# Kernel optimization log

Measured on AMD Instinct MI355X. Metric: run time of the kernel, lower is better.

Reference implementation:

```python
import jax, jax.numpy as jnp
import numpy as np

NUM_USER = 100000
NUM_ITEM = 150000
NUM_NODES = NUM_USER + NUM_ITEM
NUM_EDGES = 4000000
DIM = 64
N_LAYERS = 3
LAYER_PERM = (2, 0, 1)  # idx = [2, 0, 1] in the torch source


def setup_inputs() -> dict:
    key = jax.random.key(0)
    k1, k2 = jax.random.split(key)
    edge_index = jax.random.randint(k1, (2, NUM_EDGES), 0, NUM_NODES, dtype=jnp.int32)
    emb = jax.random.normal(k2, (NUM_NODES, DIM), dtype=jnp.float32) * 0.01  # nn.init.normal_(std=0.01)
    return {"edge_index": edge_index, "emb": emb}


def _spmm(row, col, val, feat, n):
    # out[r] = sum_{e: row[e]==r} val[e] * feat[col[e]]  -- gather + segment scatter-add
    return jax.ops.segment_sum(val[:, None] * feat[col], row, num_segments=n)


def reference(edge_index, emb):
    n = emb.shape[0]
    row, col = edge_index[0], edge_index[1]
    # dropout_node: edge-value dropout (identity in eval) + add_self_loop + bi-norm
    loop = jnp.arange(n, dtype=edge_index.dtype)
    row = jnp.concatenate([row, loop])
    col = jnp.concatenate([col, loop])
    val = jnp.ones(row.shape[0], dtype=emb.dtype)
    deg = jax.ops.segment_sum(val, row, num_segments=n)
    d_inv_sqrt = jnp.where(deg > 0, jax.lax.rsqrt(jnp.maximum(deg, 1e-12)), 0.0).astype(emb.dtype)
    val = val * d_inv_sqrt[row] * d_inv_sqrt[col]  # D^-1/2 A D^-1/2
    # n_layers of LightGCN-style SpMM propagation
    feat = emb
    feats = []
    for _ in range(N_LAYERS):
        feat = _spmm(row, col, val, feat, n)
        feats.append(feat)
    all_feat = jnp.stack(feats, axis=1)[:, jnp.array(LAYER_PERM), :]  # [N, L, D]
    return all_feat, feat
```

## Files before the change

### kernel.cpp

```cpp
#include <hip/hip_runtime.h>
#include <hip/hip_fp16.h>

#define N_NODES 250000
#define N_EDGES 4000000
#define DIM 64

#define RB_BITS 9
#define ROWS_PER_B 512
#define NB 489
#define NBPAD 512
#define P1_CHUNK 8192
#define P1_THREADS 512
#define P2_THREADS 512
#define P2_CAP 13312

#define WS_FP16_NEED 84000000ull

__device__ __forceinline__ unsigned pack2h(float a, float b) {
    unsigned ua = (unsigned)__half_as_ushort(__float2half_rn(a));
    unsigned ub = (unsigned)__half_as_ushort(__float2half_rn(b));
    return ua | (ub << 16);
}
__device__ __forceinline__ float2 unpack2h(unsigned u) {
    float a = __half2float(__ushort_as_half((unsigned short)(u & 0xffffu)));
    float b = __half2float(__ushort_as_half((unsigned short)(u >> 16)));
    return make_float2(a, b);
}

__global__ __launch_bounds__(256) void bucket_count(const int* __restrict__ row,
                                                    int* __restrict__ bcnt) {
    __shared__ int h[NBPAD];
    for (int i = threadIdx.x; i < NBPAD; i += 256) h[i] = 0;
    __syncthreads();
    int stride = gridDim.x * 256;
    for (int e4 = blockIdx.x * 256 + threadIdx.x; e4 < N_EDGES / 4; e4 += stride) {
        int4 r = ((const int4*)row)[e4];
        atomicAdd(&h[r.x >> RB_BITS], 1);
        atomicAdd(&h[r.y >> RB_BITS], 1);
        atomicAdd(&h[r.z >> RB_BITS], 1);
        atomicAdd(&h[r.w >> RB_BITS], 1);
    }
    __syncthreads();
    for (int i = threadIdx.x; i < NB; i += 256) {
        int v = h[i];
        if (v) atomicAdd(&bcnt[i], v);
    }
}

__global__ __launch_bounds__(NBPAD) void scan_buckets(const int* __restrict__ bcnt,
                                                      int* __restrict__ bbase,
                                                      int* __restrict__ bcur) {
    __shared__ int sm[NBPAD];
    int t = threadIdx.x;
    int v = (t < NB) ? bcnt[t] : 0;
    sm[t] = v;
    __syncthreads();
    for (int off = 1; off < NBPAD; off <<= 1) {
        int u = (t >= off) ? sm[t - off] : 0;
        __syncthreads();
        sm[t] += u;
        __syncthreads();
    }
    int ex = sm[t] - v;
    if (t < NB) { bbase[t] = ex; bcur[t] = ex; }
}

__global__ __launch_bounds__(P1_THREADS) void partition_edges(
        const int* __restrict__ row, const int* __restrict__ col,
        int* __restrict__ bcur, unsigned int* __restrict__ bucketed) {
    __shared__ int histo[NBPAD];
    __shared__ int base[NBPAD];
    __shared__ int cursor[NBPAD];
    __shared__ int gbase[NBPAD];
    __shared__ unsigned int staged[P1_CHUNK];
    __shared__ unsigned short stagedB[P1_CHUNK];

    int t = threadIdx.x;
    histo[t] = 0;
    __syncthreads();

    int c4base = blockIdx.x * (P1_CHUNK / 4);
    int4 r[4], c[4];
    bool val[4];
#pragma unroll
    for (int i = 0; i < 4; ++i) {
        int e4 = c4base + i * P1_THREADS + t;
        val[i] = (e4 < N_EDGES / 4);
        if (val[i]) {
            r[i] = ((const int4*)row)[e4];
            c[i] = ((const int4*)col)[e4];
            atomicAdd(&histo[r[i].x >> RB_BITS], 1);
            atomicAdd(&histo[r[i].y >> RB_BITS], 1);
            atomicAdd(&histo[r[i].z >> RB_BITS], 1);
            atomicAdd(&histo[r[i].w >> RB_BITS], 1);
        }
    }
    __syncthreads();
    int hv = histo[t];
    base[t] = hv;
    __syncthreads();
    for (int off = 1; off < NBPAD; off <<= 1) {
        int u = (t >= off) ? base[t - off] : 0;
        __syncthreads();
        base[t] += u;
        __syncthreads();
    }
    int ex = base[t] - hv;
    base[t] = ex;
    cursor[t] = ex;
    if (t < NB && hv > 0) gbase[t] = atomicAdd(&bcur[t], hv);
    __syncthreads();
#pragma unroll
    for (int i = 0; i < 4; ++i) {
        if (val[i]) {
            int rr[4] = {r[i].x, r[i].y, r[i].z, r[i].w};
            int cc[4] = {c[i].x, c[i].y, c[i].z, c[i].w};
#pragma unroll
            for (int u = 0; u < 4; ++u) {
                int b = rr[u] >> RB_BITS;
                int pos = atomicAdd(&cursor[b], 1);
                staged[pos]  = ((unsigned)(rr[u] & (ROWS_PER_B - 1)) << 18) | (unsigned)cc[u];
                stagedB[pos] = (unsigned short)b;
            }
        }
    }
    __syncthreads();
    int cnt_total = N_EDGES - blockIdx.x * P1_CHUNK;
    if (cnt_total > P1_CHUNK) cnt_total = P1_CHUNK;
    for (int s = t; s < cnt_total; s += P1_THREADS) {
        int b = stagedB[s];
        int gpos = gbase[b] + (s - base[b]);
        bucketed[gpos] = staged[s];
    }
}

__global__ __launch_bounds__(P2_THREADS) void build_csr(
        const int* __restrict__ bcnt, const int* __restrict__ bbase,
        unsigned int* csr,
        int* __restrict__ deg, int* __restrict__ row_ptr, float* __restrict__ dis) {
    __shared__ unsigned int staged[P2_CAP];
    __shared__ int histo[ROWS_PER_B];
    __shared__ int base[ROWS_PER_B];
    int b = blockIdx.x;
    int nb = bcnt[b];
    int gstart = bbase[b];
    int t = threadIdx.x;
    histo[t] = 0;
    __syncthreads();
    for (int s = t; s < nb; s += P2_THREADS) {
        unsigned int w = csr[gstart + s];
        staged[s] = w;
        atomicAdd(&histo[w >> 18], 1);
    }
    __syncthreads();
    int hv = histo[t];
    base[t] = hv;
    __syncthreads();
    for (int off = 1; off < ROWS_PER_B; off <<= 1) {
        int u = (t >= off) ? base[t - off] : 0;
        __syncthreads();
        base[t] += u;
        __syncthreads();
    }
    int ex = base[t] - hv;
    base[t] = ex;
    int node = (b << RB_BITS) + t;
    if (node < N_NODES) {
        deg[node] = hv;
        row_ptr[node] = gstart + ex;
        dis[node] = rsqrtf((float)(hv + 1));
    }
    __syncthreads();
    for (int s = t; s < nb; s += P2_THREADS) {
        unsigned int w = staged[s];
        int rl = (int)(w >> 18);
        int p = atomicAdd(&base[rl], 1);
        csr[gstart + p] = w & 0x3FFFFu;
    }
}

__global__ __launch_bounds__(256) void f32_to_f16(const float* __restrict__ in,
                                                  unsigned int* __restrict__ outh) {
    int i = blockIdx.x * blockDim.x + threadIdx.x;
    if (i < N_NODES * (DIM / 4)) {
        float4 v = ((const float4*)in)[i];
        uint2 pk;
        pk.x = pack2h(v.x, v.y);
        pk.y = pack2h(v.z, v.w);
        ((uint2*)outh)[i] = pk;
    }
}

__global__ __launch_bounds__(256) void spmm_h(const int* __restrict__ row_ptr,
                                              const int* __restrict__ deg,
                                              const int* __restrict__ csr_col,
                                              const float* __restrict__ dis,
                                              const unsigned int* __restrict__ fin_h,
                                              float* __restrict__ fout, int out_stride4, int out_off,
                                              unsigned int* __restrict__ fout_h,
                                              float* __restrict__ fout2) {
    int lane = threadIdx.x & 63;
    int lq   = lane & 15;
    int qb   = lane & 48;
    int r    = blockIdx.x * 16 + (threadIdx.x >> 4);
    if (r >= N_NODES) return;

    const uint2* fin2 = (const uint2*)fin_h;
    float dr = dis[r];
    uint2 sh = fin2[(size_t)r * 16 + lq];
    float2 s0 = unpack2h(sh.x), s1 = unpack2h(sh.y);
    float4 acc;
    acc.x = dr * s0.x; acc.y = dr * s0.y;
    acc.z = dr * s1.x; acc.w = dr * s1.y;

    int start = row_ptr[r];
    int cnt   = deg[r];
    for (int base = 0; base < cnt; base += 16) {
        int m = cnt - base; if (m > 16) m = 16;
        int cl = 0; float wl = 0.f;
        if (lq < m) {
            cl = csr_col[start + base + lq];
            wl = dis[cl];
        }
        int m4 = (m + 3) & ~3;
        for (int j = 0; j < m4; j += 4) {
            int c[4]; float w[4]; uint2 f[4];
#pragma unroll
            for (int u = 0; u < 4; ++u) {
                c[u] = __shfl(cl, qb + j + u);
                w[u] = __shfl(wl, qb + j + u);
                f[u] = fin2[(size_t)c[u] * 16 + lq];
            }
#pragma unroll
            for (int u = 0; u < 4; ++u) {
                float2 a = unpack2h(f[u].x), b = unpack2h(f[u].y);
                acc.x += w[u] * a.x;
                acc.y += w[u] * a.y;
                acc.z += w[u] * b.x;
                acc.w += w[u] * b.y;
            }
        }
    }
    float4 v;
    v.x = dr * acc.x; v.y = dr * acc.y;
    v.z = dr * acc.z; v.w = dr * acc.w;
    ((float4*)(fout + out_off))[(size_t)r * out_stride4 + lq] = v;
    if (fout_h) {
        uint2 pk;
        pk.x = pack2h(v.x, v.y);
        pk.y = pack2h(v.z, v.w);
        ((uint2*)fout_h)[(size_t)r * 16 + lq] = pk;
    }
    if (fout2) ((float4*)fout2)[(size_t)r * 16 + lq] = v;
}

__global__ __launch_bounds__(256) void spmm(const int* __restrict__ row_ptr,
                                            const int* __restrict__ deg,
                                            const int* __restrict__ csr_col,
                                            const float* __restrict__ dis,
                                            const float* __restrict__ fin, int in_stride4, int in_off,
                                            float* __restrict__ fout, int out_stride4, int out_off,
                                            float* __restrict__ fout2) {
    int lane = threadIdx.x & 63;
    int lq   = lane & 15;
    int qb   = lane & 48;
    int r    = blockIdx.x * 16 + (threadIdx.x >> 4);
    if (r >= N_NODES) return;

    const float4* fin4 = (const float4*)(fin + in_off);
    float dr = dis[r];
    float4 self = fin4[(size_t)r * in_stride4 + lq];
    float4 acc;
    acc.x = dr * self.x; acc.y = dr * self.y;
    acc.z = dr * self.z; acc.w = dr * self.w;

    int start = row_ptr[r];
    int cnt   = deg[r];
    for (int base = 0; base < cnt; base += 16) {
        int m = cnt - base; if (m > 16) m = 16;
        int cl = 0; float wl = 0.f;
        if (lq < m) {
            cl = csr_col[start + base + lq];
            wl = dis[cl];
        }
        int m4 = (m + 3) & ~3;
        for (int j = 0; j < m4; j += 4) {
            int c[4]; float w[4]; float4 f[4];
#pragma unroll
            for (int u = 0; u < 4; ++u) {
                c[u] = __shfl(cl, qb + j + u);
                w[u] = __shfl(wl, qb + j + u);
                f[u] = fin4[(size_t)c[u] * in_stride4 + lq];
            }
#pragma unroll
            for (int u = 0; u < 4; ++u) {
                acc.x += w[u] * f[u].x;
                acc.y += w[u] * f[u].y;
                acc.z += w[u] * f[u].z;
                acc.w += w[u] * f[u].w;
            }
        }
    }
    float4 v;
    v.x = dr * acc.x; v.y = dr * acc.y;
    v.z = dr * acc.z; v.w = dr * acc.w;
    ((float4*)(fout + out_off))[(size_t)r * out_stride4 + lq] = v;
    if (fout2) ((float4*)fout2)[(size_t)r * 16 + lq] = v;
}

extern "C" void kernel_launch(void* const* d_in, const int* in_sizes, int n_in,
                              void* d_out, int out_size, void* d_ws, size_t ws_size,
                              hipStream_t stream) {
    const int*   ei  = (const int*)d_in[0];
    const float* emb = (const float*)d_in[1];
    const int* row = ei;
    const int* col = ei + N_EDGES;
    float* out = (float*)d_out;

    char* ws = (char*)d_ws;
    int*   deg      = (int*)(ws + 0);
    int*   row_ptr  = (int*)(ws + 1000000);
    float* dis      = (float*)(ws + 2000000);
    int*   bcnt     = (int*)(ws + 3000000);
    int*   bbase    = (int*)(ws + 3002048);
    int*   bcur     = (int*)(ws + 3004096);
    unsigned int* csr = (unsigned int*)(ws + 4000000);
    unsigned int* bufA = (unsigned int*)(ws + 20000000);
    unsigned int* bufB = (unsigned int*)(ws + 52000000);

    hipMemsetAsync(bcnt, 0, NBPAD * sizeof(int), stream);

    bucket_count   <<<512, 256, 0, stream>>>(row, bcnt);
    scan_buckets   <<<1, NBPAD, 0, stream>>>(bcnt, bbase, bcur);
    int p1_blocks = (N_EDGES + P1_CHUNK - 1) / P1_CHUNK;
    partition_edges<<<p1_blocks, P1_THREADS, 0, stream>>>(row, col, bcur, csr);
    build_csr      <<<NB, P2_THREADS, 0, stream>>>(bcnt, bbase, csr, deg, row_ptr, dis);

    int spmm_blocks = N_NODES / 16 + 1;
    if (ws_size >= WS_FP16_NEED) {
        int cvt_blocks = (N_NODES * (DIM / 4) + 255) / 256;
        f32_to_f16<<<cvt_blocks, 256, 0, stream>>>(emb, bufB);
        spmm_h<<<spmm_blocks, 256, 0, stream>>>(row_ptr, deg, (const int*)csr, dis,
                                                bufB, out, 48, DIM, bufA, nullptr);
        spmm_h<<<spmm_blocks, 256, 0, stream>>>(row_ptr, deg, (const int*)csr, dis,
                                                bufA, out, 48, 2 * DIM, bufB, nullptr);
        spmm_h<<<spmm_blocks, 256, 0, stream>>>(row_ptr, deg, (const int*)csr, dis,
                                                bufB, out, 48, 0, nullptr, out + 48000000);
    } else {
        spmm<<<spmm_blocks, 256, 0, stream>>>(row_ptr, deg, (const int*)csr, dis,
                                              emb, 16, 0, out, 48, DIM, nullptr);
        spmm<<<spmm_blocks, 256, 0, stream>>>(row_ptr, deg, (const int*)csr, dis,
                                              out, 48, DIM, out, 48, 2 * DIM, nullptr);
        spmm<<<spmm_blocks, 256, 0, stream>>>(row_ptr, deg, (const int*)csr, dis,
                                              out, 48, 2 * DIM, out, 48, 0, out + 48000000);
    }
}
```

Before: 634.8 us.

## Use fixed-capacity bucket windows to drop the count/scan pass, unroll gathers by eight

Each row bucket now gets a fixed window of WCAP slots in an edge buffer, with cursors preset to b*WCAP. This removes the separate bucket_count pass, the scan, the memset and their launches. build_csr now reads the bucket window straight from global memory instead of staging it in LDS, and writes an out-of-place CSR buffer, which needs extra workspace. The fp16 SpMM inner gather loop is unrolled to 8 neighbours for more memory-level parallelism. The fixed windows assume no bucket exceeds 16384 edges, which holds for uniform random edges but would silently corrupt data if a bucket overflowed. The larger workspace requirement may also push execution onto the fp32 fallback.

```diff
diff --git a/kernel.cpp b/kernel.cpp
--- a/kernel.cpp
+++ b/kernel.cpp
@@ -8,13 +8,12 @@
 #define RB_BITS 9
 #define ROWS_PER_B 512
 #define NB 489
-#define NBPAD 512
+#define WCAP 16384
 #define P1_CHUNK 8192
 #define P1_THREADS 512
 #define P2_THREADS 512
-#define P2_CAP 13312
-
-#define WS_FP16_NEED 84000000ull
+
+#define WS_FP16_NEED 134000000ull
 
 __device__ __forceinline__ unsigned pack2h(float a, float b) {
     unsigned ua = (unsigned)__half_as_ushort(__float2half_rn(a));
@@ -27,51 +26,18 @@
     return make_float2(a, b);
 }
 
-__global__ __launch_bounds__(256) void bucket_count(const int* __restrict__ row,
-                                                    int* __restrict__ bcnt) {
-    __shared__ int h[NBPAD];
-    for (int i = threadIdx.x; i < NBPAD; i += 256) h[i] = 0;
-    __syncthreads();
-    int stride = gridDim.x * 256;
-    for (int e4 = blockIdx.x * 256 + threadIdx.x; e4 < N_EDGES / 4; e4 += stride) {
-        int4 r = ((const int4*)row)[e4];
-        atomicAdd(&h[r.x >> RB_BITS], 1);
-        atomicAdd(&h[r.y >> RB_BITS], 1);
-        atomicAdd(&h[r.z >> RB_BITS], 1);
-        atomicAdd(&h[r.w >> RB_BITS], 1);
-    }
-    __syncthreads();
-    for (int i = threadIdx.x; i < NB; i += 256) {
-        int v = h[i];
-        if (v) atomicAdd(&bcnt[i], v);
-    }
-}
-
-__global__ __launch_bounds__(NBPAD) void scan_buckets(const int* __restrict__ bcnt,
-                                                      int* __restrict__ bbase,
-                                                      int* __restrict__ bcur) {
-    __shared__ int sm[NBPAD];
+__global__ __launch_bounds__(512) void init_cursors(int* __restrict__ bcur) {
     int t = threadIdx.x;
-    int v = (t < NB) ? bcnt[t] : 0;
-    sm[t] = v;
-    __syncthreads();
-    for (int off = 1; off < NBPAD; off <<= 1) {
-        int u = (t >= off) ? sm[t - off] : 0;
-        __syncthreads();
-        sm[t] += u;
-        __syncthreads();
-    }
-    int ex = sm[t] - v;
-    if (t < NB) { bbase[t] = ex; bcur[t] = ex; }
+    if (t < NB) bcur[t] = t * WCAP;
 }
 
 __global__ __launch_bounds__(P1_THREADS) void partition_edges(
         const int* __restrict__ row, const int* __restrict__ col,
-        int* __restrict__ bcur, unsigned int* __restrict__ bucketed) {
-    __shared__ int histo[NBPAD];
-    __shared__ int base[NBPAD];
-    __shared__ int cursor[NBPAD];
-    __shared__ int gbase[NBPAD];
+        int* __restrict__ bcur, unsigned int* __restrict__ ebuf) {
+    __shared__ int histo[ROWS_PER_B];
+    __shared__ int base[ROWS_PER_B];
+    __shared__ int cursor[ROWS_PER_B];
+    __shared__ int gbase[ROWS_PER_B];
     __shared__ unsigned int staged[P1_CHUNK];
     __shared__ unsigned short stagedB[P1_CHUNK];
 
@@ -99,7 +65,7 @@
     int hv = histo[t];
     base[t] = hv;
     __syncthreads();
-    for (int off = 1; off < NBPAD; off <<= 1) {
+    for (int off = 1; off < ROWS_PER_B; off <<= 1) {
         int u = (t >= off) ? base[t - off] : 0;
         __syncthreads();
         base[t] += u;
@@ -130,28 +96,25 @@
     for (int s = t; s < cnt_total; s += P1_THREADS) {
         int b = stagedB[s];
         int gpos = gbase[b] + (s - base[b]);
-        bucketed[gpos] = staged[s];
+        ebuf[gpos] = staged[s];
     }
 }
 
 __global__ __launch_bounds__(P2_THREADS) void build_csr(
-        const int* __restrict__ bcnt, const int* __restrict__ bbase,
-        unsigned int* csr,
+        const int* __restrict__ bcur, const unsigned int* __restrict__ ebuf,
+        unsigned int* __restrict__ cbuf,
         int* __restrict__ deg, int* __restrict__ row_ptr, float* __restrict__ dis) {
-    __shared__ unsigned int staged[P2_CAP];
     __shared__ int histo[ROWS_PER_B];
     __shared__ int base[ROWS_PER_B];
     int b = blockIdx.x;
-    int nb = bcnt[b];
-    int gstart = bbase[b];
+    int wstart = b * WCAP;
+    int nb = bcur[b] - wstart;
+    const unsigned int* ewin = ebuf + wstart;
     int t = threadIdx.x;
     histo[t] = 0;
     __syncthreads();
-    for (int s = t; s < nb; s += P2_THREADS) {
-        unsigned int w = csr[gstart + s];
-        staged[s] = w;
-        atomicAdd(&histo[w >> 18], 1);
-    }
+    for (int s = t; s < nb; s += P2_THREADS)
+        atomicAdd(&histo[ewin[s] >> 18], 1);
     __syncthreads();
     int hv = histo[t];
     base[t] = hv;
@@ -167,15 +130,14 @@
     int node = (b << RB_BITS) + t;
     if (node < N_NODES) {
         deg[node] = hv;
-        row_ptr[node] = gstart + ex;
+        row_ptr[node] = wstart + ex;
         dis[node] = rsqrtf((float)(hv + 1));
     }
     __syncthreads();
     for (int s = t; s < nb; s += P2_THREADS) {
-        unsigned int w = staged[s];
-        int rl = (int)(w >> 18);
-        int p = atomicAdd(&base[rl], 1);
-        csr[gstart + p] = w & 0x3FFFFu;
+        unsigned int w = ewin[s];
+        int p = atomicAdd(&base[w >> 18], 1);
+        cbuf[wstart + p] = w & 0x3FFFFu;
     }
 }
 
@@ -193,7 +155,7 @@
 
 __global__ __launch_bounds__(256) void spmm_h(const int* __restrict__ row_ptr,
                                               const int* __restrict__ deg,
-                                              const int* __restrict__ csr_col,
+                                              const unsigned int* __restrict__ csr_col,
                                               const float* __restrict__ dis,
                                               const unsigned int* __restrict__ fin_h,
                                               float* __restrict__ fout, int out_stride4, int out_off,
@@ -219,25 +181,25 @@
         int m = cnt - base; if (m > 16) m = 16;
         int cl = 0; float wl = 0.f;
         if (lq < m) {
-            cl = csr_col[start + base + lq];
+            cl = (int)csr_col[start + base + lq];
             wl = dis[cl];
         }
-        int m4 = (m + 3) & ~3;
-        for (int j = 0; j < m4; j += 4) {
-            int c[4]; float w[4]; uint2 f[4];
-#pragma unroll
-            for (int u = 0; u < 4; ++u) {
+        int m8 = (m + 7) & ~7;
+        for (int j = 0; j < m8; j += 8) {
+            int c[8]; float w[8]; uint2 f[8];
+#pragma unroll
+            for (int u = 0; u < 8; ++u) {
                 c[u] = __shfl(cl, qb + j + u);
                 w[u] = __shfl(wl, qb + j + u);
                 f[u] = fin2[(size_t)c[u] * 16 + lq];
             }
 #pragma unroll
-            for (int u = 0; u < 4; ++u) {
-                float2 a = unpack2h(f[u].x), b = unpack2h(f[u].y);
+            for (int u = 0; u < 8; ++u) {
+                float2 a = unpack2h(f[u].x), bb = unpack2h(f[u].y);
                 acc.x += w[u] * a.x;
                 acc.y += w[u] * a.y;
-                acc.z += w[u] * b.x;
-                acc.w += w[u] * b.y;
+                acc.z += w[u] * bb.x;
+                acc.w += w[u] * bb.y;
             }
         }
     }
@@ -256,7 +218,7 @@
 
 __global__ __launch_bounds__(256) void spmm(const int* __restrict__ row_ptr,
                                             const int* __restrict__ deg,
-                                            const int* __restrict__ csr_col,
+                                            const unsigned int* __restrict__ csr_col,
                                             const float* __restrict__ dis,
                                             const float* __restrict__ fin, int in_stride4, int in_off,
                                             float* __restrict__ fout, int out_stride4, int out_off,
@@ -280,7 +242,7 @@
         int m = cnt - base; if (m > 16) m = 16;
         int cl = 0; float wl = 0.f;
         if (lq < m) {
-            cl = csr_col[start + base + lq];
+            cl = (int)csr_col[start + base + lq];
             wl = dis[cl];
         }
         int m4 = (m + 3) & ~3;
@@ -321,37 +283,33 @@
     int*   deg      = (int*)(ws + 0);
     int*   row_ptr  = (int*)(ws + 1000000);
     float* dis      = (float*)(ws + 2000000);
-    int*   bcnt     = (int*)(ws + 3000000);
-    int*   bbase    = (int*)(ws + 3002048);
-    int*   bcur     = (int*)(ws + 3004096);
-    unsigned int* csr = (unsigned int*)(ws + 4000000);
-    unsigned int* bufA = (unsigned int*)(ws + 20000000);
-    unsigned int* bufB = (unsigned int*)(ws + 52000000);
-
-    hipMemsetAsync(bcnt, 0, NBPAD * sizeof(int), stream);
-
-    bucket_count   <<<512, 256, 0, stream>>>(row, bcnt);
-    scan_buckets   <<<1, NBPAD, 0, stream>>>(bcnt, bbase, bcur);
+    int*   bcur     = (int*)(ws + 3000000);
+    unsigned int* ebuf = (unsigned int*)(ws + 4000000);
+    unsigned int* cbuf = (unsigned int*)(ws + 37000000);
+    unsigned int* bufA = (unsigned int*)(ws + 70000000);
+    unsigned int* bufB = (unsigned int*)(ws + 102000000);
+
+    init_cursors   <<<1, 512, 0, stream>>>(bcur);
     int p1_blocks = (N_EDGES + P1_CHUNK - 1) / P1_CHUNK;
-    partition_edges<<<p1_blocks, P1_THREADS, 0, stream>>>(row, col, bcur, csr);
-    build_csr      <<<NB, P2_THREADS, 0, stream>>>(bcnt, bbase, csr, deg, row_ptr, dis);
+    partition_edges<<<p1_blocks, P1_THREADS, 0, stream>>>(row, col, bcur, ebuf);
+    build_csr      <<<NB, P2_THREADS, 0, stream>>>(bcur, ebuf, cbuf, deg, row_ptr, dis);
 
     int spmm_blocks = N_NODES / 16 + 1;
     if (ws_size >= WS_FP16_NEED) {
         int cvt_blocks = (N_NODES * (DIM / 4) + 255) / 256;
         f32_to_f16<<<cvt_blocks, 256, 0, stream>>>(emb, bufB);
-        spmm_h<<<spmm_blocks, 256, 0, stream>>>(row_ptr, deg, (const int*)csr, dis,
+        spmm_h<<<spmm_blocks, 256, 0, stream>>>(row_ptr, deg, cbuf, dis,
                                                 bufB, out, 48, DIM, bufA, nullptr);
-        spmm_h<<<spmm_blocks, 256, 0, stream>>>(row_ptr, deg, (const int*)csr, dis,
+        spmm_h<<<spmm_blocks, 256, 0, stream>>>(row_ptr, deg, cbuf, dis,
                                                 bufA, out, 48, 2 * DIM, bufB, nullptr);
-        spmm_h<<<spmm_blocks, 256, 0, stream>>>(row_ptr, deg, (const int*)csr, dis,
+        spmm_h<<<spmm_blocks, 256, 0, stream>>>(row_ptr, deg, cbuf, dis,
                                                 bufB, out, 48, 0, nullptr, out + 48000000);
     } else {
-        spmm<<<spmm_blocks, 256, 0, stream>>>(row_ptr, deg, (const int*)csr, dis,
+        spmm<<<spmm_blocks, 256, 0, stream>>>(row_ptr, deg, cbuf, dis,
                                               emb, 16, 0, out, 48, DIM, nullptr);
-        spmm<<<spmm_blocks, 256, 0, stream>>>(row_ptr, deg, (const int*)csr, dis,
+        spmm<<<spmm_blocks, 256, 0, stream>>>(row_ptr, deg, cbuf, dis,
                                               out, 48, DIM, out, 48, 2 * DIM, nullptr);
-        spmm<<<spmm_blocks, 256, 0, stream>>>(row_ptr, deg, (const int*)csr, dis,
+        spmm<<<spmm_blocks, 256, 0, stream>>>(row_ptr, deg, cbuf, dis,
                                               out, 48, 2 * DIM, out, 48, 0, out + 48000000);
     }
 }
```

Measured after the change: 619.3 us. 2.4% less time.
